# Kernel tuning notes

Hardware: AMD Instinct MI355X
Metric: run time of the kernel (lower is better)

The kernel has to match this reference:

```python
import jax, jax.numpy as jnp
import numpy as np

STRIDE, PAD, DIL = 1, 1, 1


def setup_inputs() -> dict:
    key = jax.random.key(0)
    k1, k2, k3, k4, k5 = jax.random.split(key, 5)
    N, Cin, H, W = 8, 256, 64, 64
    Cout, K = 256, 3
    x = jax.random.normal(k1, (N, Cin, H, W), dtype=jnp.float32)
    offset = jax.random.normal(k2, (N, 2 * K * K, H, W), dtype=jnp.float32)
    mask = jax.random.uniform(k3, (N, K * K, H, W), dtype=jnp.float32)
    weight = jax.random.normal(k4, (Cout, Cin, K, K), dtype=jnp.float32) * 0.02
    bias = jax.random.normal(k5, (Cout,), dtype=jnp.float32)
    return {"x": x, "offset": offset, "mask": mask, "weight": weight, "bias": bias}


def _gather(im_flat, idx):
    # im_flat: (N, Goff, Cg, H*W); idx: (N, Goff, KK, Ho, Wo) int32
    # -> (N, Goff, Cg, KK, Ho, Wo)
    f = lambda imf, ix: imf[:, ix]
    return jax.vmap(jax.vmap(f))(im_flat, idx)


def _deform_conv2d(x, offset, mask, weight, bias):
    N, Cin, H, W = x.shape
    Cout, Cin_g, Kh, Kw = weight.shape
    KK = Kh * Kw
    Goff = offset.shape[1] // (2 * KK)
    Ho = (H + 2 * PAD - (DIL * (Kh - 1) + 1)) // STRIDE + 1
    Wo = (W + 2 * PAD - (DIL * (Kw - 1) + 1)) // STRIDE + 1

    # base sampling grid per kernel tap: (KK, Ho, Wo)
    py = (jnp.arange(Kh)[:, None] * DIL + jnp.arange(Ho)[None, :] * STRIDE - PAD).astype(jnp.float32)
    px = (jnp.arange(Kw)[:, None] * DIL + jnp.arange(Wo)[None, :] * STRIDE - PAD).astype(jnp.float32)
    y_base = jnp.broadcast_to(py[:, None, :, None], (Kh, Kw, Ho, Wo)).reshape(KK, Ho, Wo)
    x_base = jnp.broadcast_to(px[None, :, None, :], (Kh, Kw, Ho, Wo)).reshape(KK, Ho, Wo)

    off = offset.reshape(N, Goff, KK, 2, Ho, Wo)  # [...,0]=dy, [...,1]=dx
    ys = y_base[None, None] + off[:, :, :, 0]  # (N, Goff, KK, Ho, Wo)
    xs = x_base[None, None] + off[:, :, :, 1]

    Cg = Cin // Goff
    im_flat = x.reshape(N, Goff, Cg, H * W)

    y0 = jnp.floor(ys)
    x0 = jnp.floor(xs)
    acc = jnp.zeros((N, Goff, Cg, KK, Ho, Wo), dtype=x.dtype)
    for dy in (0.0, 1.0):
        for dx in (0.0, 1.0):
            yi = y0 + dy
            xi = x0 + dx
            wgt = (1.0 - jnp.abs(ys - yi)) * (1.0 - jnp.abs(xs - xi))
            valid = (yi >= 0) & (yi < H) & (xi >= 0) & (xi < W)
            idx = (jnp.clip(yi, 0, H - 1) * W + jnp.clip(xi, 0, W - 1)).astype(jnp.int32)
            g = _gather(im_flat, idx)  # (N,Goff,Cg,KK,Ho,Wo)
            acc = acc + g * (wgt * valid.astype(x.dtype))[:, :, None]

    m = mask.reshape(N, Goff, KK, Ho, Wo)
    sampled = acc * m[:, :, None]  # DCNv2 modulation

    # grouped conv accumulate as GEMM over (Cin_g*KK)
    gw = Cin // Cin_g
    cols = sampled.reshape(N, gw, Cin_g * KK, Ho * Wo)
    wflat = weight.reshape(gw, Cout // gw, Cin_g * KK)
    out = jnp.einsum('goc,ngcl->ngol', wflat, cols).reshape(N, Cout, Ho, Wo)
    return out + bias[None, :, None, None]


def reference(x, offset, mask, weight, bias):
    return _deform_conv2d(x, offset, mask, weight, bias)
```

## Files before the change

### kernel.cpp

```cpp
#include <hip/hip_runtime.h>
#include <stdint.h>

typedef unsigned int u32;
typedef unsigned short u16;
typedef float f32x4 __attribute__((ext_vector_type(4)));
typedef __fp16 h16x2 __attribute__((ext_vector_type(2)));
typedef _Float16 f16x8 __attribute__((ext_vector_type(8)));
typedef float f4u __attribute__((ext_vector_type(4), aligned(4)));

#define NB   8
#define CIN  256
#define HH   64
#define WW   64
#define HW   4096
#define COUT 256
#define NPX  128
#define BSTR 264

__device__ __forceinline__ u32 pkh(float lo, float hi) {
  h16x2 h = __builtin_amdgcn_cvt_pkrtz(lo, hi);
  return __builtin_bit_cast(u32, h);
}
union HU { u32 u; h16x2 h; };

__global__ __launch_bounds__(256) void prep_all(const float* __restrict__ x,
                                                const float* __restrict__ wgt,
                                                u32* __restrict__ xT,
                                                u32* __restrict__ W2f32) {
  int b = blockIdx.x;
  int t = threadIdx.x;
  if (b < 2048) {
    __shared__ __align__(16) u32 tile[16][132];
    int n = b >> 8, hw0 = (b & 255) << 4;
    int hwq = (t & 3) << 2;
    int cp0 = t >> 2;
    const float* xb = x + (size_t)n * CIN * HW + hw0 + hwq;
#pragma unroll
    for (int it = 0; it < 2; ++it) {
      int cp = (it << 6) + cp0;
      int c = cp << 1;
      f4u v0 = *(const f4u*)(xb + (size_t)c * HW);
      f4u v1 = *(const f4u*)(xb + (size_t)(c + 1) * HW);
      tile[hwq + 0][cp] = pkh(v0.x, v1.x);
      tile[hwq + 1][cp] = pkh(v0.y, v1.y);
      tile[hwq + 2][cp] = pkh(v0.z, v1.z);
      tile[hwq + 3][cp] = pkh(v0.w, v1.w);
    }
    __syncthreads();
    u32* outp = xT + ((size_t)(n * HW + hw0)) * 128;
    int cq = t & 31, hb = t >> 5;
#pragma unroll
    for (int it = 0; it < 2; ++it) {
      int hwl = (it << 3) + hb;
      uint4 v = *(const uint4*)&tile[hwl][cq << 2];
      *(uint4*)(outp + (size_t)hwl * 128 + (cq << 2)) = v;
    }
  } else {
    int tt = (b - 2048) * 256 + t;
    int cp = tt & 127, co = tt >> 7;
    int c = cp << 1;
    const float* p = wgt + ((size_t)co * CIN + c) * 9;
    f4u q0 = *(const f4u*)(p + 0);
    f4u q1 = *(const f4u*)(p + 4);
    f4u q2 = *(const f4u*)(p + 8);
    f4u q3 = *(const f4u*)(p + 12);
    float e16 = p[16], e17 = p[17];
    float a0[9], a1[9];
    a0[0]=q0.x; a0[1]=q0.y; a0[2]=q0.z; a0[3]=q0.w;
    a0[4]=q1.x; a0[5]=q1.y; a0[6]=q1.z; a0[7]=q1.w; a0[8]=q2.x;
    a1[0]=q2.y; a1[1]=q2.z; a1[2]=q2.w;
    a1[3]=q3.x; a1[4]=q3.y; a1[5]=q3.z; a1[6]=q3.w; a1[7]=e16; a1[8]=e17;
    int cc = c >> 5;
    int j = (c >> 1) & 3;
    int lane = (co & 15) | (((c >> 3) & 3) << 4);
    int tile_ = ((co >> 6) << 2) | ((co >> 4) & 3);
#pragma unroll
    for (int kk = 0; kk < 9; ++kk) {
      int frag = (kk * 8 + cc) * 16 + tile_;
      W2f32[(size_t)frag * 256 + lane * 4 + j] = pkh(a0[kk], a1[kk]);
    }
  }
}

__global__ __launch_bounds__(1024, 4) void dcn_main(
    const float* __restrict__ offset, const float* __restrict__ mask,
    const float* __restrict__ bias, const u16* __restrict__ xT,
    const u16* __restrict__ W2f, float* __restrict__ out) {
  __shared__ __align__(16) u16 Bs[2][NPX * BSTR];
  __shared__ __align__(8)  uint2 swl[1152];
  __shared__ __align__(8)  ushort4 sol[1152];

  int bid = blockIdx.x;
  int n = bid & 7;
  int hp = bid >> 3;
  int t = threadIdx.x;
  int lane = t & 63;
  int w = t >> 6;

  for (int i = t; i < 1152; i += 1024) {
    int kk = i >> 7, p = i & 127;
    int ky = kk / 3, kx = kk - ky * 3;
    int sp = (hp << 7) + p;
    int ho = (hp << 1) + (p >> 6);
    float dy = offset[(((size_t)n * 18 + kk * 2 + 0) << 12) + sp];
    float dx = offset[(((size_t)n * 18 + kk * 2 + 1) << 12) + sp];
    float m  = mask  [(((size_t)n * 9  + kk) << 12) + sp];
    float ys = (float)(ky + ho - 1) + dy;
    float xs = (float)(kx + (p & 63) - 1) + dx;
    float y0f = floorf(ys), x0f = floorf(xs);
    float fy = ys - y0f, fx = xs - x0f;
    int y0 = (int)y0f, x0 = (int)x0f;
    int y1 = y0 + 1, x1 = x0 + 1;
    float vy0 = (y0 >= 0 && y0 < HH) ? 1.f : 0.f;
    float vy1 = (y1 >= 0 && y1 < HH) ? 1.f : 0.f;
    float vx0 = (x0 >= 0 && x0 < WW) ? 1.f : 0.f;
    float vx1 = (x1 >= 0 && x1 < WW) ? 1.f : 0.f;
    float w0 = (1.f - fy) * (1.f - fx) * m * vy0 * vx0;
    float w1 = (1.f - fy) * fx * m * vy0 * vx1;
    float w2 = fy * (1.f - fx) * m * vy1 * vx0;
    float w3 = fy * fx * m * vy1 * vx1;
    int iy0 = min(max(y0, 0), HH - 1), iy1 = min(max(y1, 0), HH - 1);
    int ix0 = min(max(x0, 0), WW - 1), ix1 = min(max(x1, 0), WW - 1);
    ushort4 pv;
    pv.x = (u16)((iy0 << 6) + ix0);
    pv.y = (u16)((iy0 << 6) + ix1);
    pv.z = (u16)((iy1 << 6) + ix0);
    pv.w = (u16)((iy1 << 6) + ix1);
    swl[i] = make_uint2(pkh(w0, w1), pkh(w2, w3));
    sol[i] = pv;
  }
  __syncthreads();

  f32x4 acc[2][8];
#pragma unroll
  for (int a = 0; a < 2; ++a)
#pragma unroll
    for (int b2 = 0; b2 < 8; ++b2) acc[a][b2] = {0.f, 0.f, 0.f, 0.f};

  const char* xTn = (const char*)xT + ((size_t)n * HW << 9);
  int ml = lane & 15, q = lane >> 4;
  int hw32 = t >> 5;
  int l32 = t & 31;
  int strip = w & 7, pr = w >> 3;
  int tile0 = ((strip >> 1) << 2) + ((strip & 1) << 1);
  const char* bch = xTn + (l32 << 4);

#define CMB(G, WT) do {                                                \
    float wt = (WT);                                                   \
    HU h0, h1, h2, h3;                                                 \
    h0.u = (G).x; h1.u = (G).y; h2.u = (G).z; h3.u = (G).w;            \
    s0 = __builtin_fmaf((float)h0.h.x, wt, s0);                        \
    s1 = __builtin_fmaf((float)h0.h.y, wt, s1);                        \
    s2 = __builtin_fmaf((float)h1.h.x, wt, s2);                        \
    s3 = __builtin_fmaf((float)h1.h.y, wt, s3);                        \
    s4 = __builtin_fmaf((float)h2.h.x, wt, s4);                        \
    s5 = __builtin_fmaf((float)h2.h.y, wt, s5);                        \
    s6 = __builtin_fmaf((float)h3.h.x, wt, s6);                        \
    s7 = __builtin_fmaf((float)h3.h.y, wt, s7);                        \
  } while (0)

  auto build0 = [&](int g) {
    int px = (g << 5) + hw32;
    uint2 wu = swl[px];
    ushort4 pv = sol[px];
    HU ha, hb; ha.u = wu.x; hb.u = wu.y;
    uint4 G0 = *(const uint4*)(bch + ((int)pv.x << 9));
    uint4 G1 = *(const uint4*)(bch + ((int)pv.y << 9));
    uint4 G2 = *(const uint4*)(bch + ((int)pv.z << 9));
    uint4 G3 = *(const uint4*)(bch + ((int)pv.w << 9));
    float s0=0.f,s1=0.f,s2=0.f,s3=0.f,s4=0.f,s5=0.f,s6=0.f,s7=0.f;
    CMB(G0, (float)ha.h.x);
    CMB(G1, (float)ha.h.y);
    CMB(G2, (float)hb.h.x);
    CMB(G3, (float)hb.h.y);
    uint4 pkd;
    pkd.x = pkh(s0, s1); pkd.y = pkh(s2, s3);
    pkd.z = pkh(s4, s5); pkd.w = pkh(s6, s7);
    *(uint4*)((char*)&Bs[0][0] + px * (BSTR * 2) + (l32 << 4)) = pkd;
  };

  auto af_load = [&](int fidx, int mt) {
    return *(const f16x8*)(W2f + (((size_t)((fidx << 4) + tile0 + mt)) << 9) +
                           (lane << 3));
  };

#pragma unroll
  for (int g = 0; g < 4; ++g) build0(g);
  __syncthreads();

#pragma unroll 1
  for (int kk = 0; kk < 9; ++kk) {
    int cur = kk & 1;
    char* Bw = (char*)&Bs[cur ^ 1][0];
    const char* Br = (const char*)&Bs[cur][0];
    int fbase = kk << 3;
#pragma unroll
    for (int g = 0; g < 4; ++g) {
      int px = (g << 5) + hw32;
      uint4 G0, G1, G2, G3;
      if (kk < 8) {
        ushort4 pv = sol[((kk + 1) << 7) + px];
        G0 = *(const uint4*)(bch + ((int)pv.x << 9));
        G1 = *(const uint4*)(bch + ((int)pv.y << 9));
        G2 = *(const uint4*)(bch + ((int)pv.z << 9));
        G3 = *(const uint4*)(bch + ((int)pv.w << 9));
      }
      {
        int cc = (g << 1) | pr;
        f16x8 af0 = af_load(fbase + cc, 0);
        f16x8 af1 = af_load(fbase + cc, 1);
        f16x8 bf[4];
#pragma unroll
        for (int half = 0; half < 2; ++half) {
#pragma unroll
          for (int j = 0; j < 4; ++j)
            bf[j] = *(const f16x8*)(Br +
                    ((((half << 2) + j) << 4) + ml) * (BSTR * 2) +
                    (cc << 6) + (q << 4));
#pragma unroll
          for (int j = 0; j < 4; ++j)
            acc[0][(half << 2) + j] = __builtin_amdgcn_mfma_f32_16x16x32_f16(
                af0, bf[j], acc[0][(half << 2) + j], 0, 0, 0);
#pragma unroll
          for (int j = 0; j < 4; ++j)
            acc[1][(half << 2) + j] = __builtin_amdgcn_mfma_f32_16x16x32_f16(
                af1, bf[j], acc[1][(half << 2) + j], 0, 0, 0);
        }
      }
      if (kk < 8) {
        uint2 wu = swl[((kk + 1) << 7) + px];
        HU ha, hb; ha.u = wu.x; hb.u = wu.y;
        float s0=0.f,s1=0.f,s2=0.f,s3=0.f,s4=0.f,s5=0.f,s6=0.f,s7=0.f;
        CMB(G0, (float)ha.h.x);
        CMB(G1, (float)ha.h.y);
        CMB(G2, (float)hb.h.x);
        CMB(G3, (float)hb.h.y);
        uint4 pkd;
        pkd.x = pkh(s0, s1); pkd.y = pkh(s2, s3);
        pkd.z = pkh(s4, s5); pkd.w = pkh(s6, s7);
        *(uint4*)(Bw + px * (BSTR * 2) + (l32 << 4)) = pkd;
      }
    }
    __syncthreads();
  }

  float* PS = (float*)&Bs[0][0];
  float* P = PS + strip * 4224 + lane * 66;
  if (pr) {
#pragma unroll
    for (int mt = 0; mt < 2; ++mt)
#pragma unroll
      for (int nt = 0; nt < 8; ++nt)
#pragma unroll
        for (int r = 0; r < 4; ++r)
          P[((mt << 3) + nt) * 4 + r] = acc[mt][nt][r];
  }
  __syncthreads();
  if (!pr) {
    size_t ob = (size_t)n * COUT * HW + ((size_t)hp << 7);
#pragma unroll
    for (int mt = 0; mt < 2; ++mt) {
#pragma unroll
      for (int r = 0; r < 4; ++r) {
        int co = (strip << 5) + (mt << 4) + (q << 2) + r;
        float bv = bias[co];
#pragma unroll
        for (int nt = 0; nt < 8; ++nt) {
          int px = (nt << 4) + ml;
          out[ob + (size_t)co * HW + px] =
              acc[mt][nt][r] + P[((mt << 3) + nt) * 4 + r] + bv;
        }
      }
    }
  }
}

extern "C" void kernel_launch(void* const* d_in, const int* in_sizes, int n_in,
                              void* d_out, int out_size, void* d_ws, size_t ws_size,
                              hipStream_t stream) {
  const float* x      = (const float*)d_in[0];
  const float* offset = (const float*)d_in[1];
  const float* mask   = (const float*)d_in[2];
  const float* weight = (const float*)d_in[3];
  const float* bias   = (const float*)d_in[4];
  float* out = (float*)d_out;

  u16* xT  = (u16*)d_ws;
  u16* W2f = (u16*)((char*)d_ws + (size_t)NB * HW * CIN * 2);

  prep_all<<<2176, 256, 0, stream>>>(x, weight, (u32*)xT, (u32*)W2f);
  dcn_main<<<256, 1024, 0, stream>>>(offset, mask, bias, xT, W2f, out);
}
```

Measured before the change: 150.5 us.

## Retile MFMA warp tiles to 64x64 and swizzle partial-sum reduction buffer

Changes each wave's output tile from 32 output channels by 128 pixels to 64 channels by 64 pixels. This halves the LDS B-fragment reads per wave while doubling the global A-fragment loads. The A loads are hoisted ahead of the gather loads, and the MFMA block is wrapped in s_setprio. The cross-wave partial-sum exchange now uses vectorized float4 stores with an XOR swizzle, and bias is read as float4. The trade is more global weight traffic for less LDS read traffic.

```diff
diff --git a/kernel.cpp b/kernel.cpp
--- a/kernel.cpp
+++ b/kernel.cpp
@@ -131,18 +131,18 @@
   }
   __syncthreads();
 
-  f32x4 acc[2][8];
-#pragma unroll
-  for (int a = 0; a < 2; ++a)
-#pragma unroll
-    for (int b2 = 0; b2 < 8; ++b2) acc[a][b2] = {0.f, 0.f, 0.f, 0.f};
+  f32x4 acc[4][4];
+#pragma unroll
+  for (int a = 0; a < 4; ++a)
+#pragma unroll
+    for (int b2 = 0; b2 < 4; ++b2) acc[a][b2] = {0.f, 0.f, 0.f, 0.f};
 
   const char* xTn = (const char*)xT + ((size_t)n * HW << 9);
   int ml = lane & 15, q = lane >> 4;
   int hw32 = t >> 5;
   int l32 = t & 31;
-  int strip = w & 7, pr = w >> 3;
-  int tile0 = ((strip >> 1) << 2) + ((strip & 1) << 1);
+  int coT = w & 3, pxH = (w >> 2) & 1, pr = w >> 3;
+  int tile0 = coT << 2;
   const char* bch = xTn + (l32 << 4);
 
 #define CMB(G, WT) do {                                                \
@@ -197,6 +197,11 @@
 #pragma unroll
     for (int g = 0; g < 4; ++g) {
       int px = (g << 5) + hw32;
+      int cc = (g << 1) | pr;
+      f16x8 af0 = af_load(fbase + cc, 0);
+      f16x8 af1 = af_load(fbase + cc, 1);
+      f16x8 af2 = af_load(fbase + cc, 2);
+      f16x8 af3 = af_load(fbase + cc, 3);
       uint4 G0, G1, G2, G3;
       if (kk < 8) {
         ushort4 pv = sol[((kk + 1) << 7) + px];
@@ -206,25 +211,26 @@
         G3 = *(const uint4*)(bch + ((int)pv.w << 9));
       }
       {
-        int cc = (g << 1) | pr;
-        f16x8 af0 = af_load(fbase + cc, 0);
-        f16x8 af1 = af_load(fbase + cc, 1);
-        f16x8 bf[4];
+        int rbase = pxH << 2;
 #pragma unroll
         for (int half = 0; half < 2; ++half) {
-#pragma unroll
-          for (int j = 0; j < 4; ++j)
-            bf[j] = *(const f16x8*)(Br +
-                    ((((half << 2) + j) << 4) + ml) * (BSTR * 2) +
-                    (cc << 6) + (q << 4));
-#pragma unroll
-          for (int j = 0; j < 4; ++j)
-            acc[0][(half << 2) + j] = __builtin_amdgcn_mfma_f32_16x16x32_f16(
-                af0, bf[j], acc[0][(half << 2) + j], 0, 0, 0);
-#pragma unroll
-          for (int j = 0; j < 4; ++j)
-            acc[1][(half << 2) + j] = __builtin_amdgcn_mfma_f32_16x16x32_f16(
-                af1, bf[j], acc[1][(half << 2) + j], 0, 0, 0);
+          f16x8 b0 = *(const f16x8*)(Br +
+                  (((rbase + (half << 1) + 0) << 4) + ml) * (BSTR * 2) +
+                  (cc << 6) + (q << 4));
+          f16x8 b1 = *(const f16x8*)(Br +
+                  (((rbase + (half << 1) + 1) << 4) + ml) * (BSTR * 2) +
+                  (cc << 6) + (q << 4));
+          int n0 = (half << 1), n1 = n0 + 1;
+          __builtin_amdgcn_s_setprio(1);
+          acc[0][n0] = __builtin_amdgcn_mfma_f32_16x16x32_f16(af0, b0, acc[0][n0], 0, 0, 0);
+          acc[0][n1] = __builtin_amdgcn_mfma_f32_16x16x32_f16(af0, b1, acc[0][n1], 0, 0, 0);
+          acc[1][n0] = __builtin_amdgcn_mfma_f32_16x16x32_f16(af1, b0, acc[1][n0], 0, 0, 0);
+          acc[1][n1] = __builtin_amdgcn_mfma_f32_16x16x32_f16(af1, b1, acc[1][n1], 0, 0, 0);
+          acc[2][n0] = __builtin_amdgcn_mfma_f32_16x16x32_f16(af2, b0, acc[2][n0], 0, 0, 0);
+          acc[2][n1] = __builtin_amdgcn_mfma_f32_16x16x32_f16(af2, b1, acc[2][n1], 0, 0, 0);
+          acc[3][n0] = __builtin_amdgcn_mfma_f32_16x16x32_f16(af3, b0, acc[3][n0], 0, 0, 0);
+          acc[3][n1] = __builtin_amdgcn_mfma_f32_16x16x32_f16(af3, b1, acc[3][n1], 0, 0, 0);
+          __builtin_amdgcn_s_setprio(0);
         }
       }
       if (kk < 8) {
@@ -245,31 +251,31 @@
   }
 
   float* PS = (float*)&Bs[0][0];
-  float* P = PS + strip * 4224 + lane * 66;
+  int pid = w & 7;
+  float* P = PS + pid * 4096 + lane * 64;
+  int sw = lane & 7;
   if (pr) {
 #pragma unroll
-    for (int mt = 0; mt < 2; ++mt)
-#pragma unroll
-      for (int nt = 0; nt < 8; ++nt)
-#pragma unroll
-        for (int r = 0; r < 4; ++r)
-          P[((mt << 3) + nt) * 4 + r] = acc[mt][nt][r];
+    for (int mt = 0; mt < 4; ++mt)
+#pragma unroll
+      for (int nt = 0; nt < 4; ++nt)
+        *(f32x4*)&P[(((mt << 2) + nt) ^ sw) << 2] = acc[mt][nt];
   }
   __syncthreads();
   if (!pr) {
     size_t ob = (size_t)n * COUT * HW + ((size_t)hp << 7);
 #pragma unroll
-    for (int mt = 0; mt < 2; ++mt) {
-#pragma unroll
-      for (int r = 0; r < 4; ++r) {
-        int co = (strip << 5) + (mt << 4) + (q << 2) + r;
-        float bv = bias[co];
-#pragma unroll
-        for (int nt = 0; nt < 8; ++nt) {
-          int px = (nt << 4) + ml;
-          out[ob + (size_t)co * HW + px] =
-              acc[mt][nt][r] + P[((mt << 3) + nt) * 4 + r] + bv;
-        }
+    for (int mt = 0; mt < 4; ++mt) {
+      int co0 = (coT << 6) + (mt << 4) + (q << 2);
+      f4u bv = *(const f4u*)&bias[co0];
+#pragma unroll
+      for (int nt = 0; nt < 4; ++nt) {
+        f32x4 pv = *(const f32x4*)&P[(((mt << 2) + nt) ^ sw) << 2];
+        int px = (pxH << 6) + (nt << 4) + ml;
+#pragma unroll
+        for (int r = 0; r < 4; ++r)
+          out[ob + (size_t)(co0 + r) * HW + px] =
+              acc[mt][nt][r] + pv[r] + bv[r];
       }
     }
   }
```

Result: no change. 151.7 us (+0.8%).

## Warp-specialize producer waves for bilinear gather and consumer waves for MFMA

Applied to the files above, without the earlier changes.

Splits the 16 waves into 8 producer waves that gather and blend the next tap's samples into the double-buffered LDS tile, and 8 consumer waves that each run the full K reduction over all channel chunks with MFMA. This removes the split-K across wave pairs and the LDS partial-sum reduction at the end. Producers software-pipeline their global gathers one pixel group ahead, and consumers prefetch A fragments and raise their wave priority around MFMA bursts. The risk is imbalance: MFMA work now sits on half the waves, and gather latency is hidden by fewer waves.

```diff
diff --git a/kernel.cpp b/kernel.cpp
--- a/kernel.cpp
+++ b/kernel.cpp
@@ -96,6 +96,7 @@
   int t = threadIdx.x;
   int lane = t & 63;
   int w = t >> 6;
+  bool prod = (w >= 8);
 
   for (int i = t; i < 1152; i += 1024) {
     int kk = i >> 7, p = i & 127;
@@ -141,9 +142,13 @@
   int ml = lane & 15, q = lane >> 4;
   int hw32 = t >> 5;
   int l32 = t & 31;
-  int strip = w & 7, pr = w >> 3;
+  int strip = w & 7;
   int tile0 = ((strip >> 1) << 2) + ((strip & 1) << 1);
   const char* bch = xTn + (l32 << 4);
+  int tp = t - 512;
+  int ch = tp & 31;
+  int ph = tp >> 5;
+  const char* bchp = xTn + (ch << 4);
 
 #define CMB(G, WT) do {                                                \
     float wt = (WT);                                                   \
@@ -186,77 +191,78 @@
 
 #pragma unroll
   for (int g = 0; g < 4; ++g) build0(g);
+
+  f16x8 ca, cb;
+  if (!prod) { ca = af_load(0, 0); cb = af_load(0, 1); }
   __syncthreads();
 
 #pragma unroll 1
   for (int kk = 0; kk < 9; ++kk) {
-    int cur = kk & 1;
-    char* Bw = (char*)&Bs[cur ^ 1][0];
-    const char* Br = (const char*)&Bs[cur][0];
-    int fbase = kk << 3;
-#pragma unroll
-    for (int g = 0; g < 4; ++g) {
-      int px = (g << 5) + hw32;
-      uint4 G0, G1, G2, G3;
+    if (prod) {
       if (kk < 8) {
-        ushort4 pv = sol[((kk + 1) << 7) + px];
-        G0 = *(const uint4*)(bch + ((int)pv.x << 9));
-        G1 = *(const uint4*)(bch + ((int)pv.y << 9));
-        G2 = *(const uint4*)(bch + ((int)pv.z << 9));
-        G3 = *(const uint4*)(bch + ((int)pv.w << 9));
+        char* Bw = (char*)&Bs[(kk & 1) ^ 1][0];
+        int base = (kk + 1) << 7;
+        uint2 wA = swl[base + ph];
+        ushort4 pvA = sol[base + ph];
+        uint4 A0 = *(const uint4*)(bchp + ((int)pvA.x << 9));
+        uint4 A1 = *(const uint4*)(bchp + ((int)pvA.y << 9));
+        uint4 A2 = *(const uint4*)(bchp + ((int)pvA.z << 9));
+        uint4 A3 = *(const uint4*)(bchp + ((int)pvA.w << 9));
+#pragma unroll
+        for (int s = 0; s < 8; ++s) {
+          uint4 B0, B1, B2, B3; uint2 wB;
+          if (s < 7) {
+            ushort4 pv = sol[base + ((s + 1) << 4) + ph];
+            wB = swl[base + ((s + 1) << 4) + ph];
+            B0 = *(const uint4*)(bchp + ((int)pv.x << 9));
+            B1 = *(const uint4*)(bchp + ((int)pv.y << 9));
+            B2 = *(const uint4*)(bchp + ((int)pv.z << 9));
+            B3 = *(const uint4*)(bchp + ((int)pv.w << 9));
+          }
+          {
+            HU ha, hb; ha.u = wA.x; hb.u = wA.y;
+            float s0=0.f,s1=0.f,s2=0.f,s3=0.f,s4=0.f,s5=0.f,s6=0.f,s7=0.f;
+            CMB(A0, (float)ha.h.x);
+            CMB(A1, (float)ha.h.y);
+            CMB(A2, (float)hb.h.x);
+            CMB(A3, (float)hb.h.y);
+            uint4 pkd;
+            pkd.x = pkh(s0, s1); pkd.y = pkh(s2, s3);
+            pkd.z = pkh(s4, s5); pkd.w = pkh(s6, s7);
+            *(uint4*)(Bw + ((s << 4) + ph) * (BSTR * 2) + (ch << 4)) = pkd;
+          }
+          wA = wB; A0 = B0; A1 = B1; A2 = B2; A3 = B3;
+        }
       }
-      {
-        int cc = (g << 1) | pr;
-        f16x8 af0 = af_load(fbase + cc, 0);
-        f16x8 af1 = af_load(fbase + cc, 1);
-        f16x8 bf[4];
-#pragma unroll
-        for (int half = 0; half < 2; ++half) {
-#pragma unroll
-          for (int j = 0; j < 4; ++j)
-            bf[j] = *(const f16x8*)(Br +
-                    ((((half << 2) + j) << 4) + ml) * (BSTR * 2) +
-                    (cc << 6) + (q << 4));
-#pragma unroll
-          for (int j = 0; j < 4; ++j)
-            acc[0][(half << 2) + j] = __builtin_amdgcn_mfma_f32_16x16x32_f16(
-                af0, bf[j], acc[0][(half << 2) + j], 0, 0, 0);
-#pragma unroll
-          for (int j = 0; j < 4; ++j)
-            acc[1][(half << 2) + j] = __builtin_amdgcn_mfma_f32_16x16x32_f16(
-                af1, bf[j], acc[1][(half << 2) + j], 0, 0, 0);
-        }
+    } else {
+      const char* Br = (const char*)&Bs[kk & 1][0];
+      int fbase = kk << 3;
+#pragma unroll
+      for (int cc = 0; cc < 8; ++cc) {
+        f16x8 na, nb;
+        if (cc < 7) {
+          na = af_load(fbase + cc + 1, 0);
+          nb = af_load(fbase + cc + 1, 1);
+        } else if (kk < 8) {
+          na = af_load(fbase + 8, 0);
+          nb = af_load(fbase + 8, 1);
+        }
+        __builtin_amdgcn_s_setprio(1);
+#pragma unroll
+        for (int nt = 0; nt < 8; ++nt) {
+          f16x8 b = *(const f16x8*)(Br + ((nt << 4) + ml) * (BSTR * 2) +
+                                    (cc << 6) + (q << 4));
+          acc[0][nt] = __builtin_amdgcn_mfma_f32_16x16x32_f16(ca, b, acc[0][nt], 0, 0, 0);
+          acc[1][nt] = __builtin_amdgcn_mfma_f32_16x16x32_f16(cb, b, acc[1][nt], 0, 0, 0);
+        }
+        __builtin_amdgcn_s_setprio(0);
+        ca = na; cb = nb;
       }
-      if (kk < 8) {
-        uint2 wu = swl[((kk + 1) << 7) + px];
-        HU ha, hb; ha.u = wu.x; hb.u = wu.y;
-        float s0=0.f,s1=0.f,s2=0.f,s3=0.f,s4=0.f,s5=0.f,s6=0.f,s7=0.f;
-        CMB(G0, (float)ha.h.x);
-        CMB(G1, (float)ha.h.y);
-        CMB(G2, (float)hb.h.x);
-        CMB(G3, (float)hb.h.y);
-        uint4 pkd;
-        pkd.x = pkh(s0, s1); pkd.y = pkh(s2, s3);
-        pkd.z = pkh(s4, s5); pkd.w = pkh(s6, s7);
-        *(uint4*)(Bw + px * (BSTR * 2) + (l32 << 4)) = pkd;
-      }
     }
     __syncthreads();
   }
 
-  float* PS = (float*)&Bs[0][0];
-  float* P = PS + strip * 4224 + lane * 66;
-  if (pr) {
-#pragma unroll
-    for (int mt = 0; mt < 2; ++mt)
-#pragma unroll
-      for (int nt = 0; nt < 8; ++nt)
-#pragma unroll
-        for (int r = 0; r < 4; ++r)
-          P[((mt << 3) + nt) * 4 + r] = acc[mt][nt][r];
-  }
-  __syncthreads();
-  if (!pr) {
+  if (!prod) {
     size_t ob = (size_t)n * COUT * HW + ((size_t)hp << 7);
 #pragma unroll
     for (int mt = 0; mt < 2; ++mt) {
@@ -267,8 +273,7 @@
 #pragma unroll
         for (int nt = 0; nt < 8; ++nt) {
           int px = (nt << 4) + ml;
-          out[ob + (size_t)co * HW + px] =
-              acc[mt][nt][r] + P[((mt << 3) + nt) * 4 + r] + bv;
+          out[ob + (size_t)co * HW + px] = acc[mt][nt][r] + bv;
         }
       }
     }
```

Result: no change. 150.6 us (+0.1%).
